# Optimization experiments

Hardware: AMD Instinct MI355X
Metric: run time of the kernel (lower is better)

## Reference

```python
import jax, jax.numpy as jnp
import numpy as np

N_NODES = 50000
N_EDGES = 800000
IN_DIM = 64
EDGE_DIM = 2
HID = 128
NUM_LAYERS = 4
NUM_GRAPHS = 128
BN_EPS = 1e-5


def setup_inputs() -> dict:
    key = jax.random.key(0)
    ks = jax.random.split(key, 24)
    s = 0.05
    inp = {
        "x": jax.random.normal(ks[0], (N_NODES, IN_DIM), jnp.float32),
        "edge_attr": jax.random.normal(ks[1], (N_EDGES, EDGE_DIM), jnp.float32),
        "edge_index": jax.random.randint(ks[2], (2, N_EDGES), 0, N_NODES, jnp.int32),
        "batch": jnp.sort(jax.random.randint(ks[3], (N_NODES,), 0, NUM_GRAPHS, jnp.int32)),
        # parameters
        "W_in": jax.random.normal(ks[4], (IN_DIM, HID), jnp.float32) * s,
        "b_in": jnp.zeros((HID,), jnp.float32),
        "W_e": jax.random.normal(ks[5], (EDGE_DIM, HID), jnp.float32) * s,
        "b_e": jnp.zeros((HID,), jnp.float32),
        "conv_W1": jax.random.normal(ks[6], (NUM_LAYERS, HID, HID), jnp.float32) * s,
        "conv_b1": jnp.zeros((NUM_LAYERS, HID), jnp.float32),
        "conv_W2": jax.random.normal(ks[7], (NUM_LAYERS, HID, HID), jnp.float32) * s,
        "conv_b2": jnp.zeros((NUM_LAYERS, HID), jnp.float32),
        "bn_g": jnp.ones((NUM_LAYERS, HID), jnp.float32),
        "bn_b": jnp.zeros((NUM_LAYERS, HID), jnp.float32),
        "vn_W1": jax.random.normal(ks[8], (HID, HID), jnp.float32) * s,
        "vn_b1": jnp.zeros((HID,), jnp.float32),
        "vn_W2": jax.random.normal(ks[9], (HID, HID), jnp.float32) * s,
        "vn_b2": jnp.zeros((HID,), jnp.float32),
        "cls_W1": jax.random.normal(ks[10], (HID, HID), jnp.float32) * s,
        "cls_b1": jnp.zeros((HID,), jnp.float32),
        "cls_W2": jax.random.normal(ks[11], (HID, 1), jnp.float32) * s,
        "cls_b2": jnp.zeros((1,), jnp.float32),
    }
    return inp


def reference(x, edge_attr, W_in, b_in, W_e, b_e, conv_W1, conv_b1, conv_W2, conv_b2,
              bn_g, bn_b, vn_W1, vn_b1, vn_W2, vn_b2, cls_W1, cls_b1, cls_W2, cls_b2,
              edge_index, batch):
    seg = jax.ops.segment_sum
    n = x.shape[0]
    src, dst = edge_index[0], edge_index[1]

    h = x @ W_in + b_in                      # [N, H]
    e = edge_attr @ W_e + b_e                # [E, H]
    vn = jnp.zeros((NUM_GRAPHS, HID), h.dtype)

    for i in range(NUM_LAYERS):
        h = h + vn[batch]                    # virtual-node broadcast
        # GINEConv (eps=0): msg = relu(x_j + e); aggregate-sum at dst; mlp(x_i + aggr)
        m = jax.nn.relu(h[src] + e)          # [E, H]
        aggr = seg(m, dst, num_segments=n)   # [N, H]
        z = h + aggr
        z = jax.nn.relu(z @ conv_W1[i] + conv_b1[i]) @ conv_W2[i] + conv_b2[i]
        # BatchNorm1d over node dim (batch statistics, biased variance)
        mu = jnp.mean(z, axis=0)
        var = jnp.mean(jnp.square(z - mu), axis=0)
        z = (z - mu) * jax.lax.rsqrt(var + BN_EPS) * bn_g[i] + bn_b[i]
        h = jax.nn.relu(z)                   # dropout disabled (deterministic)
        if i != NUM_LAYERS - 1:
            vn_up = seg(h, batch, num_segments=NUM_GRAPHS)   # global_add_pool
            vn = vn + (jax.nn.relu(vn_up @ vn_W1 + vn_b1) @ vn_W2 + vn_b2)

    # global_mean_pool
    counts = seg(jnp.ones((n,), h.dtype), batch, num_segments=NUM_GRAPHS)
    g = seg(h, batch, num_segments=NUM_GRAPHS) / jnp.maximum(counts, 1.0)[:, None]
    logits = (jax.nn.relu(g @ cls_W1 + cls_b1) @ cls_W2 + cls_b2).reshape(-1)
    return logits
```

## Files before the change

### kernel.cpp

```cpp
#include <hip/hip_runtime.h>

#define N_NODES 50000
#define N_EDGES 800000
#define IN_DIM 64
#define HID 128
#define NUM_LAYERS 4
#define NUM_GRAPHS 128
#define BN_EPS 1e-5f

typedef __attribute__((ext_vector_type(8))) short short8;
typedef __attribute__((ext_vector_type(4))) float f32x4;

__device__ inline unsigned short f2bf(float f) {
    unsigned int u = __float_as_uint(f);
    u += 0x7FFFu + ((u >> 16) & 1u);
    return (unsigned short)(u >> 16);
}
__device__ inline float bflo(unsigned int p) { return __uint_as_float(p << 16); }
__device__ inline float bfhi(unsigned int p) { return __uint_as_float(p & 0xFFFF0000u); }
__device__ inline float bfch(const uint4& v, int c) {
    unsigned int p = (&v.x)[c >> 1];
    return (c & 1) ? bfhi(p) : bflo(p);
}


__global__ void hist_kernel(const int* __restrict__ dst, int* __restrict__ cnt,
                            int* __restrict__ rank) {
    int base = blockIdx.x * 1024 + threadIdx.x;
#pragma unroll
    for (int u = 0; u < 4; ++u) {
        int e = base + u * 256;
        if (e < N_EDGES) rank[e] = atomicAdd(&cnt[dst[e]], 1);
    }
}

__global__ void endpos_kernel(const int* __restrict__ batch, int* __restrict__ endpos) {
    int n = blockIdx.x * 256 + threadIdx.x;
    if (n >= N_NODES) return;
    int b = batch[n];
    int b1 = (n + 1 < N_NODES) ? batch[n + 1] : NUM_GRAPHS;
    for (int g = b; g < b1; ++g) endpos[g] = n + 1;
    if (n == 0)
        for (int g = 0; g < b; ++g) endpos[g] = 0;
}

__global__ void wprep_kernel(const float* __restrict__ W_in,
                             const float* __restrict__ conv_W1,
                             const float* __restrict__ conv_W2,
                             unsigned short* __restrict__ wt_in,
                             unsigned short* __restrict__ wt1,
                             unsigned short* __restrict__ wt2) {
    int i = blockIdx.x * 256 + threadIdx.x;
    if (i < 128 * IN_DIM) {
        int c = i >> 6, k = i & 63;
        wt_in[i] = f2bf(W_in[k * HID + c]);
    }
    if (i < 4 * HID * HID) {
        int o = i & (HID * HID - 1);
        int layer = i >> 14;
        int c = o >> 7, k = o & 127;
        wt1[i] = f2bf(conv_W1[layer * HID * HID + k * HID + c]);
        wt2[i] = f2bf(conv_W2[layer * HID * HID + k * HID + c]);
    }
}

#define SCAN_BLOCKS ((N_NODES + 1023) / 1024)

__global__ __launch_bounds__(1024) void scan1_kernel(const int* __restrict__ cnt,
                                                     int* __restrict__ bsum) {
    __shared__ int ls[1024];
    int t = threadIdx.x;
    int g = blockIdx.x * 1024 + t;
    int v = (g < N_NODES) ? cnt[g] : 0;
    ls[t] = v;
    __syncthreads();
    for (int off = 512; off > 0; off >>= 1) {
        if (t < off) ls[t] += ls[t + off];
        __syncthreads();
    }
    if (t == 0) bsum[blockIdx.x] = ls[0];
}

__global__ void scan2_kernel(const int* __restrict__ bsum, int* __restrict__ boff) {
    if (threadIdx.x == 0) {
        int r = 0;
        for (int i = 0; i < SCAN_BLOCKS; ++i) {
            boff[i] = r;
            r += bsum[i];
        }
    }
}

__global__ __launch_bounds__(1024) void scan3_kernel(const int* __restrict__ cnt,
                                                     const int* __restrict__ boff,
                                                     int* __restrict__ row_start) {
    __shared__ int ls[1024];
    int t = threadIdx.x;
    int g = blockIdx.x * 1024 + t;
    int v = (g < N_NODES) ? cnt[g] : 0;
    ls[t] = v;
    __syncthreads();
    for (int off = 1; off < 1024; off <<= 1) {
        int x = (t >= off) ? ls[t - off] : 0;
        __syncthreads();
        ls[t] += x;
        __syncthreads();
    }
    int excl = ls[t] - v + boff[blockIdx.x];
    if (g < N_NODES) {
        row_start[g] = excl;
        if (g == N_NODES - 1) row_start[N_NODES] = excl + v;
    }
}

__global__ void fill_kernel(const int* __restrict__ src, const int* __restrict__ dst,
                            const float* __restrict__ ea, const int* __restrict__ rank,
                            const int* __restrict__ row_start, const int* __restrict__ batch,
                            int4* __restrict__ edges) {
    int e = blockIdx.x * 256 + threadIdx.x;
    if (e >= N_EDGES) return;
    float2 a = *(const float2*)&ea[2 * e];
    int s = src[e];
    int p = row_start[dst[e]] + rank[e];
    edges[p] = make_int4(s, __float_as_int(a.x), __float_as_int(a.y), batch[s]);
}

template <int HASVN>
__global__ __launch_bounds__(256) void aggr_kernel(const unsigned short* __restrict__ hbf,
                                                   const unsigned short* __restrict__ vnb,
                                                   const int* __restrict__ batch,
                                                   const int4* __restrict__ edges,
                                                   const int* __restrict__ row_start,
                                                   const float* __restrict__ We,
                                                   const float* __restrict__ be,
                                                   unsigned short* __restrict__ zbf,
                                                   float* __restrict__ S1,
                                                   float* __restrict__ S2) {
    int tid = threadIdx.x;
    if (blockIdx.x == 0 && tid < HID) {
        S1[tid] = 0.f;
        S2[tid] = 0.f;
    }
    int cg = (tid & 15) * 8;
    int n = blockIdx.x * 16 + (tid >> 4);

    float w0[8], w1[8], bc[8];
    {
        float4 a0 = *(const float4*)&We[cg], a1 = *(const float4*)&We[cg + 4];
        float4 b0 = *(const float4*)&We[HID + cg], b1v = *(const float4*)&We[HID + cg + 4];
        float4 c0 = *(const float4*)&be[cg], c1 = *(const float4*)&be[cg + 4];
        w0[0]=a0.x; w0[1]=a0.y; w0[2]=a0.z; w0[3]=a0.w; w0[4]=a1.x; w0[5]=a1.y; w0[6]=a1.z; w0[7]=a1.w;
        w1[0]=b0.x; w1[1]=b0.y; w1[2]=b0.z; w1[3]=b0.w; w1[4]=b1v.x; w1[5]=b1v.y; w1[6]=b1v.z; w1[7]=b1v.w;
        bc[0]=c0.x; bc[1]=c0.y; bc[2]=c0.z; bc[3]=c0.w; bc[4]=c1.x; bc[5]=c1.y; bc[6]=c1.z; bc[7]=c1.w;
    }

    float s[8];
    {
        uint4 hs = *(const uint4*)&hbf[(size_t)n * HID + cg];
#pragma unroll
        for (int c = 0; c < 8; ++c) s[c] = bfch(hs, c);
        if (HASVN) {
            uint4 vs = *(const uint4*)&vnb[(size_t)batch[n] * HID + cg];
#pragma unroll
            for (int c = 0; c < 8; ++c) s[c] += bfch(vs, c);
        }
    }

    int jb = row_start[n], je = row_start[n + 1];
    float acc[8];
#pragma unroll
    for (int c = 0; c < 8; ++c) acc[c] = 0.f;

    int j = jb;
    for (; j + 4 <= je; j += 4) {
        int4 q[4];
        uint4 hq[4], vq[4];
#pragma unroll
        for (int u = 0; u < 4; ++u) q[u] = edges[j + u];
#pragma unroll
        for (int u = 0; u < 4; ++u) hq[u] = *(const uint4*)&hbf[(size_t)q[u].x * HID + cg];
        if (HASVN) {
#pragma unroll
            for (int u = 0; u < 4; ++u) vq[u] = *(const uint4*)&vnb[(size_t)q[u].w * HID + cg];
        }
#pragma unroll
        for (int u = 0; u < 4; ++u) {
            float ex = __int_as_float(q[u].y), ey = __int_as_float(q[u].z);
#pragma unroll
            for (int c = 0; c < 8; ++c) {
                float hv = bfch(hq[u], c);
                if (HASVN) hv += bfch(vq[u], c);
                acc[c] += fmaxf(hv + fmaf(ex, w0[c], fmaf(ey, w1[c], bc[c])), 0.f);
            }
        }
    }
    for (; j < je; ++j) {
        int4 q = edges[j];
        uint4 hq = *(const uint4*)&hbf[(size_t)q.x * HID + cg];
        uint4 vq;
        if (HASVN) vq = *(const uint4*)&vnb[(size_t)q.w * HID + cg];
        float ex = __int_as_float(q.y), ey = __int_as_float(q.z);
#pragma unroll
        for (int c = 0; c < 8; ++c) {
            float hv = bfch(hq, c);
            if (HASVN) hv += bfch(vq, c);
            acc[c] += fmaxf(hv + fmaf(ex, w0[c], fmaf(ey, w1[c], bc[c])), 0.f);
        }
    }

    unsigned int o[4];
#pragma unroll
    for (int p = 0; p < 4; ++p)
        o[p] = (unsigned int)f2bf(s[2 * p] + acc[2 * p]) |
               ((unsigned int)f2bf(s[2 * p + 1] + acc[2 * p + 1]) << 16);
    *(uint4*)&zbf[(size_t)n * HID + cg] = make_uint4(o[0], o[1], o[2], o[3]);
}

__global__ __launch_bounds__(256) void ingemm_kernel(const float* __restrict__ A,
                                                     const unsigned short* __restrict__ Wt,
                                                     const float* __restrict__ bias,
                                                     unsigned short* __restrict__ outbf) {
    constexpr int KD = IN_DIM;
    __shared__ unsigned short aS[64 * KD];
    __shared__ unsigned short wS[128 * KD];
    int tid = threadIdx.x;
    int row0 = blockIdx.x * 64;

#pragma unroll
    for (int it = 0; it < (64 * KD) / (256 * 4); ++it) {
        int idx = it * 1024 + tid * 4;
        int r = idx / KD, k = idx % KD;
        int grow = row0 + r;
        float4 v = (grow < N_NODES) ? *(const float4*)&A[(size_t)grow * KD + k]
                                    : make_float4(0.f, 0.f, 0.f, 0.f);
        unsigned int d0 = (unsigned int)f2bf(v.x) | ((unsigned int)f2bf(v.y) << 16);
        unsigned int d1 = (unsigned int)f2bf(v.z) | ((unsigned int)f2bf(v.w) << 16);
        unsigned int byte = (unsigned int)(idx * 2) ^ (unsigned int)((r & 7) << 4);
        *(uint2*)((char*)aS + byte) = make_uint2(d0, d1);
    }
#pragma unroll
    for (int it = 0; it < (128 * KD) / (256 * 8); ++it) {
        int idx = it * 2048 + tid * 8;
        int c = idx / KD;
        uint4 v = *(const uint4*)&Wt[idx];
        unsigned int byte = (unsigned int)(idx * 2) ^ (unsigned int)((c & 7) << 4);
        *(uint4*)((char*)wS + byte) = v;
    }
    __syncthreads();

    int w = tid >> 6, l = tid & 63;
    int wr = w >> 1, wc = w & 1, lr = l & 15, kq = (l >> 4) * 8;
    f32x4 acc[2][4];
#pragma unroll
    for (int r = 0; r < 2; ++r)
#pragma unroll
        for (int t = 0; t < 4; ++t) acc[r][t] = (f32x4){0.f, 0.f, 0.f, 0.f};

#pragma unroll
    for (int sstep = 0; sstep < KD / 32; ++sstep) {
        int k0 = sstep * 32 + kq;
        int ar0 = 32 * wr + lr, ar1 = ar0 + 16;
        short8 af0 = *(short8*)((char*)aS + ((unsigned int)((ar0 * KD + k0) * 2) ^
                                            (unsigned int)((ar0 & 7) << 4)));
        short8 af1 = *(short8*)((char*)aS + ((unsigned int)((ar1 * KD + k0) * 2) ^
                                            (unsigned int)((ar1 & 7) << 4)));
#pragma unroll
        for (int t = 0; t < 4; ++t) {
            int col = 64 * wc + 16 * t + lr;
            short8 bf = *(short8*)((char*)wS + ((unsigned int)((col * KD + k0) * 2) ^
                                               (unsigned int)((col & 7) << 4)));
            acc[0][t] = __builtin_amdgcn_mfma_f32_16x16x32_bf16(af0, bf, acc[0][t], 0, 0, 0);
            acc[1][t] = __builtin_amdgcn_mfma_f32_16x16x32_bf16(af1, bf, acc[1][t], 0, 0, 0);
        }
    }
#pragma unroll
    for (int r = 0; r < 2; ++r) {
        int rbase = row0 + 32 * wr + 16 * r + (l >> 4) * 4;
#pragma unroll
        for (int t = 0; t < 4; ++t) {
            int col = 64 * wc + 16 * t + lr;
            float b = bias[col];
#pragma unroll
            for (int q = 0; q < 4; ++q) {
                int grow = rbase + q;
                if (grow < N_NODES) outbf[(size_t)grow * HID + col] = f2bf(acc[r][t][q] + b);
            }
        }
    }
}

__global__ __launch_bounds__(256) void conv_kernel(const unsigned short* __restrict__ zbf,
                                                   const unsigned short* __restrict__ Wt1,
                                                   const float* __restrict__ b1,
                                                   const unsigned short* __restrict__ Wt2,
                                                   const float* __restrict__ b2,
                                                   float* __restrict__ B,
                                                   float* __restrict__ S1,
                                                   float* __restrict__ S2,
                                                   float* __restrict__ zinit, int zinit_n) {
    constexpr int KD = HID;
    __shared__ unsigned short aS[64 * KD];
    __shared__ unsigned short wS[128 * KD];
    __shared__ float sh1[HID], sh2[HID];
    int tid = threadIdx.x;
    if (zinit && blockIdx.x == 0)
        for (int i = tid; i < zinit_n; i += 256) zinit[i] = 0.f;
    if (tid < HID) { sh1[tid] = 0.f; sh2[tid] = 0.f; }

    int row0 = blockIdx.x * 64;

#pragma unroll
    for (int it = 0; it < 4; ++it) {
        int idx = it * 2048 + tid * 8;
        int r = idx >> 7;
        int grow = row0 + r;
        uint4 v = (grow < N_NODES) ? *(const uint4*)&zbf[(size_t)grow * HID + (idx & 127)]
                                   : make_uint4(0u, 0u, 0u, 0u);
        unsigned int byte = (unsigned int)(idx * 2) ^ (unsigned int)((r & 7) << 4);
        *(uint4*)((char*)aS + byte) = v;
    }
#pragma unroll
    for (int it = 0; it < 8; ++it) {
        int idx = it * 2048 + tid * 8;
        int c = idx >> 7;
        uint4 v = *(const uint4*)&Wt1[idx];
        unsigned int byte = (unsigned int)(idx * 2) ^ (unsigned int)((c & 7) << 4);
        *(uint4*)((char*)wS + byte) = v;
    }
    __syncthreads();

    int w = tid >> 6, l = tid & 63;
    int wr = w >> 1, wc = w & 1, lr = l & 15, kq = (l >> 4) * 8;
    int ar0 = 32 * wr + lr, ar1 = ar0 + 16;

    f32x4 acc[2][4];
#pragma unroll
    for (int r = 0; r < 2; ++r)
#pragma unroll
        for (int t = 0; t < 4; ++t) acc[r][t] = (f32x4){0.f, 0.f, 0.f, 0.f};

#pragma unroll
    for (int sstep = 0; sstep < 4; ++sstep) {
        int k0 = sstep * 32 + kq;
        short8 af0 = *(short8*)((char*)aS + ((unsigned int)((ar0 * KD + k0) * 2) ^
                                            (unsigned int)((ar0 & 7) << 4)));
        short8 af1 = *(short8*)((char*)aS + ((unsigned int)((ar1 * KD + k0) * 2) ^
                                            (unsigned int)((ar1 & 7) << 4)));
#pragma unroll
        for (int t = 0; t < 4; ++t) {
            int col = 64 * wc + 16 * t + lr;
            short8 bf = *(short8*)((char*)wS + ((unsigned int)((col * KD + k0) * 2) ^
                                               (unsigned int)((col & 7) << 4)));
            acc[0][t] = __builtin_amdgcn_mfma_f32_16x16x32_bf16(af0, bf, acc[0][t], 0, 0, 0);
            acc[1][t] = __builtin_amdgcn_mfma_f32_16x16x32_bf16(af1, bf, acc[1][t], 0, 0, 0);
        }
    }
    __syncthreads();

#pragma unroll
    for (int r = 0; r < 2; ++r) {
        int lrow0 = 32 * wr + 16 * r + (l >> 4) * 4;
#pragma unroll
        for (int t = 0; t < 4; ++t) {
            int col = 64 * wc + 16 * t + lr;
            float b = b1[col];
#pragma unroll
            for (int q = 0; q < 4; ++q) {
                int lrow = lrow0 + q;
                float v = fmaxf(acc[r][t][q] + b, 0.f);
                unsigned int byte = (unsigned int)((lrow * KD + col) * 2) ^
                                    (unsigned int)((lrow & 7) << 4);
                *(unsigned short*)((char*)aS + byte) = f2bf(v);
            }
        }
    }
#pragma unroll
    for (int it = 0; it < 8; ++it) {
        int idx = it * 2048 + tid * 8;
        int c = idx >> 7;
        uint4 v = *(const uint4*)&Wt2[idx];
        unsigned int byte = (unsigned int)(idx * 2) ^ (unsigned int)((c & 7) << 4);
        *(uint4*)((char*)wS + byte) = v;
    }
    __syncthreads();

    f32x4 acc2[2][4];
#pragma unroll
    for (int r = 0; r < 2; ++r)
#pragma unroll
        for (int t = 0; t < 4; ++t) acc2[r][t] = (f32x4){0.f, 0.f, 0.f, 0.f};

#pragma unroll
    for (int sstep = 0; sstep < 4; ++sstep) {
        int k0 = sstep * 32 + kq;
        short8 af0 = *(short8*)((char*)aS + ((unsigned int)((ar0 * KD + k0) * 2) ^
                                            (unsigned int)((ar0 & 7) << 4)));
        short8 af1 = *(short8*)((char*)aS + ((unsigned int)((ar1 * KD + k0) * 2) ^
                                            (unsigned int)((ar1 & 7) << 4)));
#pragma unroll
        for (int t = 0; t < 4; ++t) {
            int col = 64 * wc + 16 * t + lr;
            short8 bf = *(short8*)((char*)wS + ((unsigned int)((col * KD + k0) * 2) ^
                                               (unsigned int)((col & 7) << 4)));
            acc2[0][t] = __builtin_amdgcn_mfma_f32_16x16x32_bf16(af0, bf, acc2[0][t], 0, 0, 0);
            acc2[1][t] = __builtin_amdgcn_mfma_f32_16x16x32_bf16(af1, bf, acc2[1][t], 0, 0, 0);
        }
    }

#pragma unroll
    for (int r = 0; r < 2; ++r) {
        int rbase = row0 + 32 * wr + 16 * r + (l >> 4) * 4;
#pragma unroll
        for (int t = 0; t < 4; ++t) {
            int col = 64 * wc + 16 * t + lr;
            float b = b2[col];
            float s1 = 0.f, s2 = 0.f;
#pragma unroll
            for (int q = 0; q < 4; ++q) {
                int grow = rbase + q;
                if (grow < N_NODES) {
                    float v = acc2[r][t][q] + b;
                    B[(size_t)grow * HID + col] = v;
                    s1 += v;
                    s2 += v * v;
                }
            }
            atomicAdd(&sh1[col], s1);
            atomicAdd(&sh2[col], s2);
        }
    }
    __syncthreads();
    if (tid < HID) {
        atomicAdd(&S1[tid], sh1[tid]);
        atomicAdd(&S2[tid], sh2[tid]);
    }
}

__global__ __launch_bounds__(256) void bn_kernel(const float* __restrict__ z2,
                                                 const float* __restrict__ S1,
                                                 const float* __restrict__ S2,
                                                 const float* __restrict__ gma,
                                                 const float* __restrict__ bta,
                                                 const int* __restrict__ batch,
                                                 unsigned short* __restrict__ hbf,
                                                 float* __restrict__ up) {
    int tid = threadIdx.x;
    int cg = (tid & 31) * 4;
    int n0 = (blockIdx.x * 8 + (tid >> 5)) * 16;
    const float inv = 1.f / (float)N_NODES;
    float4 s1 = *(const float4*)&S1[cg];
    float4 s2 = *(const float4*)&S2[cg];
    float4 g4 = *(const float4*)&gma[cg];
    float4 b4 = *(const float4*)&bta[cg];
    float mux = s1.x * inv, muy = s1.y * inv, muz = s1.z * inv, muw = s1.w * inv;
    float gmx = g4.x * rsqrtf(s2.x * inv - mux * mux + BN_EPS);
    float gmy = g4.y * rsqrtf(s2.y * inv - muy * muy + BN_EPS);
    float gmz = g4.z * rsqrtf(s2.z * inv - muz * muz + BN_EPS);
    float gmw = g4.w * rsqrtf(s2.w * inv - muw * muw + BN_EPS);

    float4 acc = make_float4(0.f, 0.f, 0.f, 0.f);
    int gcur = -1;
    for (int i = 0; i < 16; ++i) {
        int n = n0 + i;
        if (n >= N_NODES) break;
        float4 v = *(const float4*)&z2[(size_t)n * HID + cg];
        float4 hn;
        hn.x = fmaxf(fmaf(v.x - mux, gmx, b4.x), 0.f);
        hn.y = fmaxf(fmaf(v.y - muy, gmy, b4.y), 0.f);
        hn.z = fmaxf(fmaf(v.z - muz, gmz, b4.z), 0.f);
        hn.w = fmaxf(fmaf(v.w - muw, gmw, b4.w), 0.f);
        uint2 pk;
        pk.x = (unsigned int)f2bf(hn.x) | ((unsigned int)f2bf(hn.y) << 16);
        pk.y = (unsigned int)f2bf(hn.z) | ((unsigned int)f2bf(hn.w) << 16);
        *(uint2*)&hbf[(size_t)n * HID + cg] = pk;
        int gb = batch[n];
        if (gb != gcur) {
            if (gcur >= 0) {
                atomicAdd(&up[gcur * HID + cg + 0], acc.x);
                atomicAdd(&up[gcur * HID + cg + 1], acc.y);
                atomicAdd(&up[gcur * HID + cg + 2], acc.z);
                atomicAdd(&up[gcur * HID + cg + 3], acc.w);
            }
            acc = make_float4(0.f, 0.f, 0.f, 0.f);
            gcur = gb;
        }
        acc.x += hn.x; acc.y += hn.y; acc.z += hn.z; acc.w += hn.w;
    }
    if (gcur >= 0) {
        atomicAdd(&up[gcur * HID + cg + 0], acc.x);
        atomicAdd(&up[gcur * HID + cg + 1], acc.y);
        atomicAdd(&up[gcur * HID + cg + 2], acc.z);
        atomicAdd(&up[gcur * HID + cg + 3], acc.w);
    }
}

__global__ __launch_bounds__(128) void vnmlp_kernel(const float* __restrict__ up,
                                                    const float* __restrict__ W1,
                                                    const float* __restrict__ b1,
                                                    const float* __restrict__ W2,
                                                    const float* __restrict__ b2,
                                                    float* __restrict__ vn,
                                                    unsigned short* __restrict__ vnb) {
    __shared__ float t[HID];
    int g = blockIdx.x, c = threadIdx.x;
    float s = b1[c];
#pragma unroll 8
    for (int k = 0; k < HID; ++k) s = fmaf(up[g * HID + k], W1[k * HID + c], s);
    t[c] = fmaxf(s, 0.f);
    __syncthreads();
    float s2 = b2[c];
#pragma unroll 8
    for (int k = 0; k < HID; ++k) s2 = fmaf(t[k], W2[k * HID + c], s2);
    float nv = vn[g * HID + c] + s2;
    vn[g * HID + c] = nv;
    vnb[g * HID + c] = f2bf(nv);
}

__global__ __launch_bounds__(128) void cls_kernel(const float* __restrict__ pool,
                                                  const int* __restrict__ endpos,
                                                  const float* __restrict__ W1,
                                                  const float* __restrict__ b1,
                                                  const float* __restrict__ W2,
                                                  const float* __restrict__ b2,
                                                  float* __restrict__ out) {
    __shared__ float t[HID];
    __shared__ float red[HID];
    int g = blockIdx.x, c = threadIdx.x;
    int cnt = endpos[g] - (g > 0 ? endpos[g - 1] : 0);
    float cntf = fmaxf((float)cnt, 1.f);
    t[c] = pool[g * HID + c] / cntf;
    __syncthreads();
    float s = b1[c];
#pragma unroll 8
    for (int k = 0; k < HID; ++k) s = fmaf(t[k], W1[k * HID + c], s);
    float y = fmaxf(s, 0.f);
    red[c] = y * W2[c];
    __syncthreads();
    for (int off = 64; off > 0; off >>= 1) {
        if (c < off) red[c] += red[c + off];
        __syncthreads();
    }
    if (c == 0) out[g] = red[0] + b2[0];
}

extern "C" void kernel_launch(void* const* d_in, const int* in_sizes, int n_in,
                              void* d_out, int out_size, void* d_ws, size_t ws_size,
                              hipStream_t stream) {
    const float* x        = (const float*)d_in[0];
    const float* edge_attr= (const float*)d_in[1];
    const int*   edge_idx = (const int*)d_in[2];
    const int*   batch    = (const int*)d_in[3];
    const float* W_in     = (const float*)d_in[4];
    const float* b_in     = (const float*)d_in[5];
    const float* W_e      = (const float*)d_in[6];
    const float* b_e      = (const float*)d_in[7];
    const float* conv_W1  = (const float*)d_in[8];
    const float* conv_b1  = (const float*)d_in[9];
    const float* conv_W2  = (const float*)d_in[10];
    const float* conv_b2  = (const float*)d_in[11];
    const float* bn_g     = (const float*)d_in[12];
    const float* bn_b     = (const float*)d_in[13];
    const float* vn_W1    = (const float*)d_in[14];
    const float* vn_b1    = (const float*)d_in[15];
    const float* vn_W2    = (const float*)d_in[16];
    const float* vn_b2    = (const float*)d_in[17];
    const float* cls_W1   = (const float*)d_in[18];
    const float* cls_b1   = (const float*)d_in[19];
    const float* cls_W2   = (const float*)d_in[20];
    const float* cls_b2   = (const float*)d_in[21];

    char* ws = (char*)d_ws;
    size_t off = 0;
    auto alloc = [&](size_t bytes) -> void* {
        void* p = ws + off;
        off = (off + bytes + 255) & ~(size_t)255;
        return p;
    };
    float* B = (float*)alloc((size_t)N_NODES * HID * 4);
    unsigned short* hbf = (unsigned short*)alloc((size_t)N_NODES * HID * 2);
    unsigned short* zbf = (unsigned short*)alloc((size_t)N_NODES * HID * 2);
    size_t zero_begin = off;
    int*   cnt    = (int*)alloc((size_t)N_NODES * 4);
    float* vn     = (float*)alloc((size_t)NUM_GRAPHS * HID * 4);
    unsigned short* vnb = (unsigned short*)alloc((size_t)NUM_GRAPHS * HID * 2);
    float* pool   = (float*)alloc((size_t)NUM_GRAPHS * HID * 4);
    size_t zero_end = off;
    int*    endpos    = (int*)alloc((size_t)NUM_GRAPHS * 4);
    int*    row_start = (int*)alloc((size_t)(N_NODES + 1) * 4);
    int*    rank      = (int*)alloc((size_t)N_EDGES * 4);
    int4*   edges     = (int4*)alloc((size_t)N_EDGES * 16);
    float*  vn_up     = (float*)alloc((size_t)NUM_GRAPHS * HID * 4);
    float*  S1        = (float*)alloc((size_t)HID * 4);
    float*  S2        = (float*)alloc((size_t)HID * 4);
    int*    bsum      = (int*)alloc((size_t)SCAN_BLOCKS * 4);
    int*    boff      = (int*)alloc((size_t)SCAN_BLOCKS * 4);
    unsigned short* wt_in = (unsigned short*)alloc((size_t)HID * IN_DIM * 2);
    unsigned short* wt1   = (unsigned short*)alloc((size_t)NUM_LAYERS * HID * HID * 2);
    unsigned short* wt2   = (unsigned short*)alloc((size_t)NUM_LAYERS * HID * HID * 2);
    (void)ws_size; (void)in_sizes; (void)n_in; (void)out_size;

    const int* srcp = edge_idx;
    const int* dstp = edge_idx + N_EDGES;

    hipMemsetAsync(ws + zero_begin, 0, zero_end - zero_begin, stream);
    hist_kernel<<<(N_EDGES + 1023) / 1024, 256, 0, stream>>>(dstp, cnt, rank);
    endpos_kernel<<<(N_NODES + 255) / 256, 256, 0, stream>>>(batch, endpos);
    wprep_kernel<<<(4 * HID * HID + 255) / 256, 256, 0, stream>>>(W_in, conv_W1, conv_W2,
                                                                  wt_in, wt1, wt2);
    scan1_kernel<<<SCAN_BLOCKS, 1024, 0, stream>>>(cnt, bsum);
    scan2_kernel<<<1, 64, 0, stream>>>(bsum, boff);
    scan3_kernel<<<SCAN_BLOCKS, 1024, 0, stream>>>(cnt, boff, row_start);
    fill_kernel<<<(N_EDGES + 255) / 256, 256, 0, stream>>>(srcp, dstp, edge_attr, rank,
                                                           row_start, batch, edges);

    const int gemm_grid = (N_NODES + 63) / 64;
    ingemm_kernel<<<gemm_grid, 256, 0, stream>>>(x, wt_in, b_in, hbf);

    for (int i = 0; i < NUM_LAYERS; ++i) {
        if (i == 0)
            aggr_kernel<0><<<N_NODES / 16, 256, 0, stream>>>(hbf, vnb, batch, edges, row_start,
                                                             W_e, b_e, zbf, S1, S2);
        else
            aggr_kernel<1><<<N_NODES / 16, 256, 0, stream>>>(hbf, vnb, batch, edges, row_start,
                                                             W_e, b_e, zbf, S1, S2);
        conv_kernel<<<gemm_grid, 256, 0, stream>>>(
            zbf, wt1 + (size_t)i * HID * HID, conv_b1 + (size_t)i * HID,
            wt2 + (size_t)i * HID * HID, conv_b2 + (size_t)i * HID,
            B, S1, S2, (i < NUM_LAYERS - 1) ? vn_up : nullptr, NUM_GRAPHS * HID);
        bn_kernel<<<(N_NODES + 127) / 128, 256, 0, stream>>>(B, S1, S2, bn_g + (size_t)i * HID,
                                                             bn_b + (size_t)i * HID, batch, hbf,
                                                             (i < NUM_LAYERS - 1) ? vn_up : pool);
        if (i < NUM_LAYERS - 1)
            vnmlp_kernel<<<NUM_GRAPHS, 128, 0, stream>>>(vn_up, vn_W1, vn_b1, vn_W2, vn_b2,
                                                         vn, vnb);
    }

    cls_kernel<<<NUM_GRAPHS, 128, 0, stream>>>(pool, endpos, cls_W1, cls_b1, cls_W2, cls_b2,
                                               (float*)d_out);
}
```

Before: 525.0 us.

## Precompute h+vn table before aggregation, unroll edge loop by 8, prefetch W2

A separate hvadd kernel writes h + vn[batch] to a bf16 table once per layer. The aggregation kernel then gathers a single row per edge instead of two, and batch no longer needs to be stored in the edge records. The edge loop is unrolled to 8 to keep more gathers in flight, and the conv kernel loads the second weight matrix into registers before the first GEMM so that latency overlaps. The cost is an extra kernel launch and one extra pass over the node table per layer. Rounding h+vn to bf16 before the edge sum also changes numerics slightly.

```diff
diff --git a/kernel.cpp b/kernel.cpp
--- a/kernel.cpp
+++ b/kernel.cpp
@@ -115,20 +115,35 @@
 
 __global__ void fill_kernel(const int* __restrict__ src, const int* __restrict__ dst,
                             const float* __restrict__ ea, const int* __restrict__ rank,
-                            const int* __restrict__ row_start, const int* __restrict__ batch,
-                            int4* __restrict__ edges) {
+                            const int* __restrict__ row_start, int4* __restrict__ edges) {
     int e = blockIdx.x * 256 + threadIdx.x;
     if (e >= N_EDGES) return;
     float2 a = *(const float2*)&ea[2 * e];
-    int s = src[e];
     int p = row_start[dst[e]] + rank[e];
-    edges[p] = make_int4(s, __float_as_int(a.x), __float_as_int(a.y), batch[s]);
-}
-
-template <int HASVN>
-__global__ __launch_bounds__(256) void aggr_kernel(const unsigned short* __restrict__ hbf,
-                                                   const unsigned short* __restrict__ vnb,
-                                                   const int* __restrict__ batch,
+    edges[p] = make_int4(src[e], __float_as_int(a.x), __float_as_int(a.y), 0);
+}
+
+__global__ void hvadd_kernel(const unsigned short* __restrict__ hbf,
+                             const unsigned short* __restrict__ vnb,
+                             const int* __restrict__ batch,
+                             unsigned short* __restrict__ gbf) {
+    int idx = blockIdx.x * 256 + threadIdx.x;
+    int n = idx >> 4;
+    if (n >= N_NODES) return;
+    int cg = (idx & 15) * 8;
+    uint4 h = *(const uint4*)&hbf[(size_t)n * HID + cg];
+    uint4 v = *(const uint4*)&vnb[(size_t)batch[n] * HID + cg];
+    unsigned int o[4];
+#pragma unroll
+    for (int p = 0; p < 4; ++p) {
+        float lo = bflo((&h.x)[p]) + bflo((&v.x)[p]);
+        float hi = bfhi((&h.x)[p]) + bfhi((&v.x)[p]);
+        o[p] = (unsigned int)f2bf(lo) | ((unsigned int)f2bf(hi) << 16);
+    }
+    *(uint4*)&gbf[(size_t)n * HID + cg] = make_uint4(o[0], o[1], o[2], o[3]);
+}
+
+__global__ __launch_bounds__(256) void aggr_kernel(const unsigned short* __restrict__ gbf,
                                                    const int4* __restrict__ edges,
                                                    const int* __restrict__ row_start,
                                                    const float* __restrict__ We,
@@ -154,65 +169,58 @@
         bc[0]=c0.x; bc[1]=c0.y; bc[2]=c0.z; bc[3]=c0.w; bc[4]=c1.x; bc[5]=c1.y; bc[6]=c1.z; bc[7]=c1.w;
     }
 
-    float s[8];
-    {
-        uint4 hs = *(const uint4*)&hbf[(size_t)n * HID + cg];
-#pragma unroll
-        for (int c = 0; c < 8; ++c) s[c] = bfch(hs, c);
-        if (HASVN) {
-            uint4 vs = *(const uint4*)&vnb[(size_t)batch[n] * HID + cg];
-#pragma unroll
-            for (int c = 0; c < 8; ++c) s[c] += bfch(vs, c);
-        }
-    }
-
+    uint4 hs = *(const uint4*)&gbf[(size_t)n * HID + cg];
     int jb = row_start[n], je = row_start[n + 1];
     float acc[8];
 #pragma unroll
     for (int c = 0; c < 8; ++c) acc[c] = 0.f;
 
     int j = jb;
-    for (; j + 4 <= je; j += 4) {
+    for (; j + 8 <= je; j += 8) {
+        int4 q[8];
+        uint4 hq[8];
+#pragma unroll
+        for (int u = 0; u < 8; ++u) q[u] = edges[j + u];
+#pragma unroll
+        for (int u = 0; u < 8; ++u) hq[u] = *(const uint4*)&gbf[(size_t)q[u].x * HID + cg];
+#pragma unroll
+        for (int u = 0; u < 8; ++u) {
+            float ex = __int_as_float(q[u].y), ey = __int_as_float(q[u].z);
+#pragma unroll
+            for (int c = 0; c < 8; ++c)
+                acc[c] += fmaxf(bfch(hq[u], c) + fmaf(ex, w0[c], fmaf(ey, w1[c], bc[c])), 0.f);
+        }
+    }
+    if (j + 4 <= je) {
         int4 q[4];
-        uint4 hq[4], vq[4];
+        uint4 hq[4];
 #pragma unroll
         for (int u = 0; u < 4; ++u) q[u] = edges[j + u];
 #pragma unroll
-        for (int u = 0; u < 4; ++u) hq[u] = *(const uint4*)&hbf[(size_t)q[u].x * HID + cg];
-        if (HASVN) {
-#pragma unroll
-            for (int u = 0; u < 4; ++u) vq[u] = *(const uint4*)&vnb[(size_t)q[u].w * HID + cg];
-        }
+        for (int u = 0; u < 4; ++u) hq[u] = *(const uint4*)&gbf[(size_t)q[u].x * HID + cg];
 #pragma unroll
         for (int u = 0; u < 4; ++u) {
             float ex = __int_as_float(q[u].y), ey = __int_as_float(q[u].z);
 #pragma unroll
-            for (int c = 0; c < 8; ++c) {
-                float hv = bfch(hq[u], c);
-                if (HASVN) hv += bfch(vq[u], c);
-                acc[c] += fmaxf(hv + fmaf(ex, w0[c], fmaf(ey, w1[c], bc[c])), 0.f);
-            }
-        }
+            for (int c = 0; c < 8; ++c)
+                acc[c] += fmaxf(bfch(hq[u], c) + fmaf(ex, w0[c], fmaf(ey, w1[c], bc[c])), 0.f);
+        }
+        j += 4;
     }
     for (; j < je; ++j) {
         int4 q = edges[j];
-        uint4 hq = *(const uint4*)&hbf[(size_t)q.x * HID + cg];
-        uint4 vq;
-        if (HASVN) vq = *(const uint4*)&vnb[(size_t)q.w * HID + cg];
+        uint4 hq = *(const uint4*)&gbf[(size_t)q.x * HID + cg];
         float ex = __int_as_float(q.y), ey = __int_as_float(q.z);
 #pragma unroll
-        for (int c = 0; c < 8; ++c) {
-            float hv = bfch(hq, c);
-            if (HASVN) hv += bfch(vq, c);
-            acc[c] += fmaxf(hv + fmaf(ex, w0[c], fmaf(ey, w1[c], bc[c])), 0.f);
-        }
+        for (int c = 0; c < 8; ++c)
+            acc[c] += fmaxf(bfch(hq, c) + fmaf(ex, w0[c], fmaf(ey, w1[c], bc[c])), 0.f);
     }
 
     unsigned int o[4];
 #pragma unroll
     for (int p = 0; p < 4; ++p)
-        o[p] = (unsigned int)f2bf(s[2 * p] + acc[2 * p]) |
-               ((unsigned int)f2bf(s[2 * p + 1] + acc[2 * p + 1]) << 16);
+        o[p] = (unsigned int)f2bf(bflo((&hs.x)[p]) + acc[2 * p]) |
+               ((unsigned int)f2bf(bfhi((&hs.x)[p]) + acc[2 * p + 1]) << 16);
     *(uint4*)&zbf[(size_t)n * HID + cg] = make_uint4(o[0], o[1], o[2], o[3]);
 }
 
@@ -327,6 +335,9 @@
         unsigned int byte = (unsigned int)(idx * 2) ^ (unsigned int)((c & 7) << 4);
         *(uint4*)((char*)wS + byte) = v;
     }
+    uint4 w2r[8];
+#pragma unroll
+    for (int it = 0; it < 8; ++it) w2r[it] = *(const uint4*)&Wt2[it * 2048 + tid * 8];
     __syncthreads();
 
     int w = tid >> 6, l = tid & 63;
@@ -378,9 +389,8 @@
     for (int it = 0; it < 8; ++it) {
         int idx = it * 2048 + tid * 8;
         int c = idx >> 7;
-        uint4 v = *(const uint4*)&Wt2[idx];
         unsigned int byte = (unsigned int)(idx * 2) ^ (unsigned int)((c & 7) << 4);
-        *(uint4*)((char*)wS + byte) = v;
+        *(uint4*)((char*)wS + byte) = w2r[it];
     }
     __syncthreads();
 
@@ -578,6 +588,7 @@
     };
     float* B = (float*)alloc((size_t)N_NODES * HID * 4);
     unsigned short* hbf = (unsigned short*)alloc((size_t)N_NODES * HID * 2);
+    unsigned short* gbf = (unsigned short*)alloc((size_t)N_NODES * HID * 2);
     unsigned short* zbf = (unsigned short*)alloc((size_t)N_NODES * HID * 2);
     size_t zero_begin = off;
     int*   cnt    = (int*)alloc((size_t)N_NODES * 4);
@@ -611,18 +622,19 @@
     scan2_kernel<<<1, 64, 0, stream>>>(bsum, boff);
     scan3_kernel<<<SCAN_BLOCKS, 1024, 0, stream>>>(cnt, boff, row_start);
     fill_kernel<<<(N_EDGES + 255) / 256, 256, 0, stream>>>(srcp, dstp, edge_attr, rank,
-                                                           row_start, batch, edges);
+                                                           row_start, edges);
 
     const int gemm_grid = (N_NODES + 63) / 64;
     ingemm_kernel<<<gemm_grid, 256, 0, stream>>>(x, wt_in, b_in, hbf);
 
     for (int i = 0; i < NUM_LAYERS; ++i) {
-        if (i == 0)
-            aggr_kernel<0><<<N_NODES / 16, 256, 0, stream>>>(hbf, vnb, batch, edges, row_start,
-                                                             W_e, b_e, zbf, S1, S2);
-        else
-            aggr_kernel<1><<<N_NODES / 16, 256, 0, stream>>>(hbf, vnb, batch, edges, row_start,
-                                                             W_e, b_e, zbf, S1, S2);
+        const unsigned short* src_tab = hbf;
+        if (i > 0) {
+            hvadd_kernel<<<(N_NODES * 16 + 255) / 256, 256, 0, stream>>>(hbf, vnb, batch, gbf);
+            src_tab = gbf;
+        }
+        aggr_kernel<<<N_NODES / 16, 256, 0, stream>>>(src_tab, edges, row_start,
+                                                      W_e, b_e, zbf, S1, S2);
         conv_kernel<<<gemm_grid, 256, 0, stream>>>(
             zbf, wt1 + (size_t)i * HID * HID, conv_b1 + (size_t)i * HID,
             wt2 + (size_t)i * HID * HID, conv_b2 + (size_t)i * HID,
```

New measurement: 523.7 us. Within noise of the previous version (-0.2%).
